# Performance work log

Measured on AMD Instinct MI355X. Metric: run time of the kernel, lower is better.

The kernel has to match this reference:

```python
import jax, jax.numpy as jnp
import numpy as np

N, P, C, T, V = 32, 6, 128, 64, 25
S = 3        # num_subset
CI = 32      # inter_channels
EPS = 1e-5
NEG_SLOPE = 0.1


def conv1x1(x, w, b):
    # x: (N,P,Cin,T,V), w: (Cout,Cin), b: (Cout,)
    return jnp.einsum('npctv,oc->npotv', x, w) + b[None, None, :, None, None]


def batchnorm(x, gamma, beta):
    # training-mode BN over (N,P,T,V) per channel, matching torch forward math
    mu = x.mean(axis=(0, 1, 3, 4), keepdims=True)
    var = x.var(axis=(0, 1, 3, 4), keepdims=True)
    xh = (x - mu) * jax.lax.rsqrt(var + EPS)
    return xh * gamma[None, None, :, None, None] + beta[None, None, :, None, None]


def leaky(x):
    return jnp.where(x >= 0, x, NEG_SLOPE * x)


def t_block(inp, att_bias, alphat, w_in, b_in, w_out, b_out, g_out, be_out,
            w_ff, b_ff, g_ff, be_ff):
    n, p, c, t, v = inp.shape
    qk = conv1x1(inp, w_in, b_in)                       # (N,P,2*S*CI,T,V)
    qk = qk.reshape(n, p, 2, S, CI, t, v).transpose(2, 0, 3, 1, 4, 5, 6)
    q, k = qk[0], qk[1]                                 # (N,S,P,CI,T,V)
    scores = jnp.einsum('nspctv,nspcqv->nsptq', q, k) / (CI * v)
    att = att_bias + jnp.tanh(scores) * alphat          # (N,S,P,T,T)
    y = jnp.einsum('npctv,nsptq->nspcqv', inp, att)     # (N,S,P,C,T,V)
    y = y.transpose(0, 2, 1, 3, 4, 5).reshape(n, p, S * c, t, v)
    y = batchnorm(conv1x1(y, w_out, b_out), g_out, be_out)
    y = leaky(inp + y)                                  # residual (identity down path)
    y2 = batchnorm(conv1x1(y, w_ff, b_ff), g_ff, be_ff)
    return leaky(y + y2)


def setup_inputs() -> dict:
    key = jax.random.key(0)
    ks = jax.random.split(key, 8)
    sc = 0.05
    return {
        'x': jax.random.normal(ks[0], (N, P, C, T, V), jnp.float32),
        'att_t1': jnp.zeros((1, S, 1, T, T), jnp.float32),
        'att_t2': jnp.zeros((1, S, 1, T, T), jnp.float32),
        'alphat': jnp.ones((1, S, 1, 1, 1), jnp.float32),
        'w_in': jax.random.normal(ks[1], (2 * S * CI, C), jnp.float32) * sc,
        'b_in': jax.random.normal(ks[2], (2 * S * CI,), jnp.float32) * sc,
        'w_out': jax.random.normal(ks[3], (C, S * C), jnp.float32) * sc,
        'b_out': jax.random.normal(ks[4], (C,), jnp.float32) * sc,
        'g_out': jnp.ones((C,), jnp.float32),
        'be_out': jnp.zeros((C,), jnp.float32),
        'w_ff': jax.random.normal(ks[5], (C, C), jnp.float32) * sc,
        'b_ff': jax.random.normal(ks[6], (C,), jnp.float32) * sc,
        'g_ff': jnp.ones((C,), jnp.float32),
        'be_ff': jnp.zeros((C,), jnp.float32),
    }


def reference(x, att_t1, att_t2, alphat, w_in, b_in, w_out, b_out, g_out,
              be_out, w_ff, b_ff, g_ff, be_ff):
    y = t_block(x, att_t1, alphat, w_in, b_in, w_out, b_out, g_out, be_out,
                w_ff, b_ff, g_ff, be_ff)
    z = t_block(y, att_t2, alphat, w_in, b_in, w_out, b_out, g_out, be_out,
                w_ff, b_ff, g_ff, be_ff)
    return z
```

## Files before the change

### kernel.cpp

```cpp
#include <hip/hip_runtime.h>
#include <hip/hip_bf16.h>
#include <math.h>

#define NPB  192
#define CCH  128
#define TT   64
#define VV   25
#define PIX  1600
#define SS   3
#define EPC  307200.0f
static const size_t ETOT = (size_t)NPB * CCH * PIX;

typedef __attribute__((ext_vector_type(4))) float f32x4;
typedef __attribute__((ext_vector_type(8))) short short8;

__device__ __forceinline__ ushort f2bf(float f) {
    __hip_bfloat16 h = __float2bfloat16(f);
    return __builtin_bit_cast(unsigned short, h);
}
__device__ __forceinline__ float bf2f(ushort u) {
    unsigned int x = ((unsigned int)u) << 16;
    return __builtin_bit_cast(float, x);
}

__global__ void wprep(const float* __restrict__ w_in, const float* __restrict__ b_in,
                      const float* __restrict__ w_out, const float* __restrict__ w_ff,
                      ushort* __restrict__ Wp, float* __restrict__ bp,
                      ushort* __restrict__ Wo, ushort* __restrict__ Wf) {
    int i = blockIdx.x * 256 + threadIdx.x;
    if (i < 192 * 128) {
        int r = i >> 7, c = i & 127;
        int s = r / 64, j = r % 64;
        int src = (j < 32) ? (s * 32 + j) : (96 + s * 32 + (j - 32));
        Wp[i] = f2bf(w_in[src * 128 + c]);
        if (c == 0) bp[r] = b_in[src];
    }
    if (i < 128 * 384) Wo[i] = f2bf(w_out[i]);
    if (i < 128 * 128) Wf[i] = f2bf(w_ff[i]);
}

__global__ void remap_x(const float* __restrict__ x, ushort* __restrict__ xr) {
    size_t o = ((size_t)blockIdx.x * 256 + threadIdx.x) * 4;
    size_t row = o / PIX;
    int p = (int)(o % PIX);
    int v = p >> 6, t0 = p & 63;
    const float* xp = x + row * PIX;
    uint2 u;
    u.x = (uint)f2bf(xp[(t0 + 0) * 25 + v]) | ((uint)f2bf(xp[(t0 + 1) * 25 + v]) << 16);
    u.y = (uint)f2bf(xp[(t0 + 2) * 25 + v]) | ((uint)f2bf(xp[(t0 + 3) * 25 + v]) << 16);
    *(uint2*)(xr + o) = u;
}

__global__ __launch_bounds__(256)
void gemm_conv(const void* __restrict__ inp, int in_bf16,
               const ushort* __restrict__ W, int ldw,
               const float* __restrict__ bias,
               void* __restrict__ outp, int out_bf16, int out_ch,
               int accflag)
{
    __shared__ ushort Wt[64 * 72];
    __shared__ ushort Xt[128 * 72];
    const int np = blockIdx.x;
    const int pixbase = blockIdx.y * 128;
    const int obase = blockIdx.z * 64;
    const int tid = threadIdx.x;
    const int wave = tid >> 6, lane = tid & 63;
    const int quad = lane >> 4, l16 = lane & 15;
    const int wPix = wave * 32;

    f32x4 acc[4][2];
    if (accflag) {
        const float* op = (const float*)outp + ((size_t)np * out_ch + obase) * PIX + pixbase;
#pragma unroll
        for (int ms = 0; ms < 4; ++ms)
#pragma unroll
            for (int ns = 0; ns < 2; ++ns) {
                int pl = wPix + ns * 16 + l16;
                bool valid = (pixbase + pl) < PIX;
#pragma unroll
                for (int r = 0; r < 4; ++r) {
                    int ol = ms * 16 + quad * 4 + r;
                    acc[ms][ns][r] = valid ? op[(size_t)ol * PIX + pl] : 0.f;
                }
            }
    } else {
#pragma unroll
        for (int ms = 0; ms < 4; ++ms) {
            float bv[4];
#pragma unroll
            for (int r = 0; r < 4; ++r) {
                int ol = ms * 16 + quad * 4 + r;
                bv[r] = bias ? bias[obase + ol] : 0.f;
            }
#pragma unroll
            for (int ns = 0; ns < 2; ++ns)
#pragma unroll
                for (int r = 0; r < 4; ++r) acc[ms][ns][r] = bv[r];
        }
    }

    const ushort* inb = (const ushort*)inp;
    const float* inf = (const float*)inp;
    const size_t in_off = (size_t)np * 128 * PIX;

    for (int kc = 0; kc < 2; ++kc) {
        const int kbase = kc * 64;
        {
            int o = tid >> 2, seg = tid & 3;
            const ushort* src = W + (size_t)(obase + o) * ldw + kbase + seg * 16;
            uint4 a = *(const uint4*)src;
            uint4 b = *(const uint4*)(src + 8);
            *(uint4*)&Wt[o * 72 + seg * 16] = a;
            *(uint4*)&Wt[o * 72 + seg * 16 + 8] = b;
        }
        {
            int cp = tid & 31, rq = tid >> 5;
            int c = cp * 2;
            int p0 = rq * 16;
            bool valid = (pixbase + p0) < PIX;
            if (in_bf16) {
                uint ra[8], rb[8];
                if (valid) {
                    const ushort* s0 = inb + in_off + (size_t)(kbase + c) * PIX + pixbase + p0;
                    const ushort* s1 = s0 + PIX;
                    *(uint4*)&ra[0] = *(const uint4*)s0;
                    *(uint4*)&ra[4] = *(const uint4*)(s0 + 8);
                    *(uint4*)&rb[0] = *(const uint4*)s1;
                    *(uint4*)&rb[4] = *(const uint4*)(s1 + 8);
                } else {
#pragma unroll
                    for (int h = 0; h < 8; ++h) { ra[h] = 0; rb[h] = 0; }
                }
#pragma unroll
                for (int h = 0; h < 8; ++h) {
                    uint lo = ra[h], hi = rb[h];
                    *(uint*)&Xt[(p0 + 2 * h) * 72 + c] = (lo & 0xffffu) | (hi << 16);
                    *(uint*)&Xt[(p0 + 2 * h + 1) * 72 + c] = (lo >> 16) | (hi & 0xffff0000u);
                }
            } else {
                if (valid) {
                    const float* s0 = inf + in_off + (size_t)(kbase + c) * PIX + pixbase + p0;
                    const float* s1 = s0 + PIX;
#pragma unroll
                    for (int b4 = 0; b4 < 4; ++b4) {
                        float4 u = ((const float4*)s0)[b4];
                        float4 w4 = ((const float4*)s1)[b4];
                        int p = p0 + b4 * 4;
                        *(uint*)&Xt[(p + 0) * 72 + c] = (uint)f2bf(u.x) | ((uint)f2bf(w4.x) << 16);
                        *(uint*)&Xt[(p + 1) * 72 + c] = (uint)f2bf(u.y) | ((uint)f2bf(w4.y) << 16);
                        *(uint*)&Xt[(p + 2) * 72 + c] = (uint)f2bf(u.z) | ((uint)f2bf(w4.z) << 16);
                        *(uint*)&Xt[(p + 3) * 72 + c] = (uint)f2bf(u.w) | ((uint)f2bf(w4.w) << 16);
                    }
                } else {
#pragma unroll
                    for (int h = 0; h < 16; ++h) *(uint*)&Xt[(p0 + h) * 72 + c] = 0;
                }
            }
        }
        __syncthreads();
#pragma unroll
        for (int ks = 0; ks < 2; ++ks) {
            const int kk = ks * 32;
            short8 a[4], b[2];
#pragma unroll
            for (int ms = 0; ms < 4; ++ms)
                a[ms] = *(const short8*)&Wt[(ms * 16 + l16) * 72 + kk + quad * 8];
#pragma unroll
            for (int ns = 0; ns < 2; ++ns)
                b[ns] = *(const short8*)&Xt[(wPix + ns * 16 + l16) * 72 + kk + quad * 8];
#pragma unroll
            for (int ms = 0; ms < 4; ++ms)
#pragma unroll
                for (int ns = 0; ns < 2; ++ns)
                    acc[ms][ns] = __builtin_amdgcn_mfma_f32_16x16x32_bf16(a[ms], b[ns], acc[ms][ns], 0, 0, 0);
        }
        __syncthreads();
    }

    if (out_bf16) {
        ushort* op = (ushort*)outp + ((size_t)np * out_ch + obase) * PIX + pixbase;
#pragma unroll
        for (int ms = 0; ms < 4; ++ms)
#pragma unroll
            for (int ns = 0; ns < 2; ++ns) {
                int pl = wPix + ns * 16 + l16;
                if (pixbase + pl >= PIX) continue;
#pragma unroll
                for (int r = 0; r < 4; ++r) {
                    int ol = ms * 16 + quad * 4 + r;
                    op[(size_t)ol * PIX + pl] = f2bf(acc[ms][ns][r]);
                }
            }
    } else {
        float* op = (float*)outp + ((size_t)np * out_ch + obase) * PIX + pixbase;
#pragma unroll
        for (int ms = 0; ms < 4; ++ms)
#pragma unroll
            for (int ns = 0; ns < 2; ++ns) {
                int pl = wPix + ns * 16 + l16;
                if (pixbase + pl >= PIX) continue;
#pragma unroll
                for (int r = 0; r < 4; ++r) {
                    int ol = ms * 16 + quad * 4 + r;
                    op[(size_t)ol * PIX + pl] = acc[ms][ns][r];
                }
            }
    }
}

__global__ __launch_bounds__(256)
void scores_mfma(const ushort* __restrict__ qk, const float* __restrict__ attb,
                 const float* __restrict__ alphat, ushort* __restrict__ attq)
{
    __shared__ ushort Qs[64 * 128];
    __shared__ ushort Ks[64 * 128];
    const int np = blockIdx.x, s = blockIdx.y, tid = threadIdx.x;
    const int wave = tid >> 6, lane = tid & 63;
    const int quad = lane >> 4, l16 = lane & 15;
    const int qW = (wave >> 1) * 32, tW = (wave & 1) * 32;
    const ushort* qb = qk + ((size_t)np * 192 + s * 64) * PIX;
    const ushort* kb = qb + (size_t)32 * PIX;

    const int side = wave >> 1;
    const int cil = (wave & 1) * 2 + (lane >> 5);
    const int t0 = (lane & 31) * 2;
    const ushort* sbase = (side ? kb : qb);
    ushort* dst = side ? Ks : Qs;

    f32x4 acc[2][2];
#pragma unroll
    for (int ms = 0; ms < 2; ++ms)
#pragma unroll
        for (int ns = 0; ns < 2; ++ns)
#pragma unroll
            for (int r = 0; r < 4; ++r) acc[ms][ns][r] = 0.f;

    for (int c = 0; c < 8; ++c) {
        __syncthreads();
        {
            const int ci = c * 4 + cil;
            const ushort* sb = sbase + (size_t)ci * PIX + t0;
            uint u[25];
#pragma unroll
            for (int v = 0; v < 25; ++v)
                u[v] = *(const uint*)(sb + v * 64);
            uint rA[16], rB[16];
#pragma unroll
            for (int w2 = 0; w2 < 12; ++w2) {
                uint a = u[2 * w2], b = u[2 * w2 + 1];
                rA[w2] = (a & 0xffffu) | (b << 16);
                rB[w2] = (a >> 16) | (b & 0xffff0000u);
            }
            rA[12] = u[24] & 0xffffu;  rB[12] = u[24] >> 16;
            rA[13] = 0u; rA[14] = 0u; rA[15] = 0u;
            rB[13] = 0u; rB[14] = 0u; rB[15] = 0u;
#pragma unroll
            for (int b4 = 0; b4 < 4; ++b4) {
                int blkA = (cil * 4 + b4) ^ (t0 & 7);
                int blkB = (cil * 4 + b4) ^ ((t0 + 1) & 7);
                uint4 wa, wb;
                wa.x = rA[b4 * 4 + 0]; wa.y = rA[b4 * 4 + 1];
                wa.z = rA[b4 * 4 + 2]; wa.w = rA[b4 * 4 + 3];
                wb.x = rB[b4 * 4 + 0]; wb.y = rB[b4 * 4 + 1];
                wb.z = rB[b4 * 4 + 2]; wb.w = rB[b4 * 4 + 3];
                *(uint4*)&dst[t0 * 128 + blkA * 8] = wa;
                *(uint4*)&dst[(t0 + 1) * 128 + blkB * 8] = wb;
            }
        }
        __syncthreads();
#pragma unroll
        for (int ks = 0; ks < 4; ++ks) {
            short8 a[2], b[2];
#pragma unroll
            for (int ms = 0; ms < 2; ++ms) {
                int q = qW + ms * 16 + l16;
                int blk = (ks * 4 + quad) ^ (q & 7);
                a[ms] = *(const short8*)&Ks[q * 128 + blk * 8];
            }
#pragma unroll
            for (int ns = 0; ns < 2; ++ns) {
                int t = tW + ns * 16 + l16;
                int blk = (ks * 4 + quad) ^ (t & 7);
                b[ns] = *(const short8*)&Qs[t * 128 + blk * 8];
            }
#pragma unroll
            for (int ms = 0; ms < 2; ++ms)
#pragma unroll
                for (int ns = 0; ns < 2; ++ns)
                    acc[ms][ns] = __builtin_amdgcn_mfma_f32_16x16x32_bf16(a[ms], b[ns], acc[ms][ns], 0, 0, 0);
        }
    }

    const float alpha = alphat[s];
    const int n = np / 6, p = np % 6;
    const float* bp2 = attb + (size_t)s * 4096;
    ushort* ap = attq + ((size_t)(n * SS + s) * 6 + p) * 4096;
    const float inv = 1.0f / 800.0f;
#pragma unroll
    for (int ms = 0; ms < 2; ++ms)
#pragma unroll
        for (int ns = 0; ns < 2; ++ns) {
            int t = tW + ns * 16 + l16;
#pragma unroll
            for (int r = 0; r < 4; ++r) {
                int q = qW + ms * 16 + quad * 4 + r;
                ap[q * 64 + t] = f2bf(bp2[t * 64 + q] + tanhf(acc[ms][ns][r] * inv) * alpha);
            }
        }
}

__global__ __launch_bounds__(256, 4)
void attn_conv(const ushort* __restrict__ xr, const ushort* __restrict__ attq,
               const ushort* __restrict__ Wo, const float* __restrict__ bias,
               float* __restrict__ Z)
{
    __shared__ ushort Xa[128 * 64];
    __shared__ ushort Ta[64 * 64];
    __shared__ ushort Ys[64 * 128];
    const int np = blockIdx.x, v = blockIdx.y;
    const int tid = threadIdx.x;
    const int wave = tid >> 6, lane = tid & 63;
    const int quad = lane >> 4, l16 = lane & 15;
    const int mH = (wave & 1) * 64;
    const int oH = (wave & 1) * 64;
    const int qH = (wave >> 1) * 32;
    const int n = np / 6, p = np % 6;

    {
        int cc = tid >> 1, half = tid & 1;
        const ushort* src = xr + ((size_t)np * 128 + cc) * PIX + v * 64 + half * 32;
        uint4 a = *(const uint4*)src;
        uint4 b = *(const uint4*)(src + 8);
        uint4 c0 = *(const uint4*)(src + 16);
        uint4 d = *(const uint4*)(src + 24);
        int sw = cc & 7;
        ushort* xb = &Xa[cc * 64];
        *(uint4*)&xb[((half * 4 + 0) ^ sw) * 8] = a;
        *(uint4*)&xb[((half * 4 + 1) ^ sw) * 8] = b;
        *(uint4*)&xb[((half * 4 + 2) ^ sw) * 8] = c0;
        *(uint4*)&xb[((half * 4 + 3) ^ sw) * 8] = d;
    }

    f32x4 acc2[4][2];
#pragma unroll
    for (int ms2 = 0; ms2 < 4; ++ms2) {
        float bv[4];
#pragma unroll
        for (int r = 0; r < 4; ++r)
            bv[r] = bias[oH + ms2 * 16 + quad * 4 + r];
#pragma unroll
        for (int ns = 0; ns < 2; ++ns)
#pragma unroll
            for (int r = 0; r < 4; ++r) acc2[ms2][ns][r] = bv[r];
    }

    const size_t abase = ((size_t)(n * SS) * 6 + p) * 4096;

    for (int s = 0; s < SS; ++s) {
        __syncthreads();
        {
            int r0 = tid >> 2, seg = tid & 3;
            const ushort* src = attq + abase + (size_t)s * 6 * 4096 + r0 * 64 + seg * 16;
            uint4 a = *(const uint4*)src;
            uint4 b = *(const uint4*)(src + 8);
            int sw = r0 & 7;
            ushort* tb = &Ta[r0 * 64];
            *(uint4*)&tb[((seg * 2 + 0) ^ sw) * 8] = a;
            *(uint4*)&tb[((seg * 2 + 1) ^ sw) * 8] = b;
        }
        __syncthreads();
        f32x4 acc[4][2];
#pragma unroll
        for (int ms = 0; ms < 4; ++ms)
#pragma unroll
            for (int ns = 0; ns < 2; ++ns)
#pragma unroll
                for (int r = 0; r < 4; ++r) acc[ms][ns][r] = 0.f;
#pragma unroll
        for (int ks = 0; ks < 2; ++ks) {
            short8 a[4], b[2];
#pragma unroll
            for (int ms = 0; ms < 4; ++ms) {
                int row = mH + ms * 16 + l16;
                int blk = (ks * 4 + quad) ^ (l16 & 7);
                a[ms] = *(const short8*)&Xa[row * 64 + blk * 8];
            }
#pragma unroll
            for (int ns = 0; ns < 2; ++ns) {
                int row = qH + ns * 16 + l16;
                int blk = (ks * 4 + quad) ^ (l16 & 7);
                b[ns] = *(const short8*)&Ta[row * 64 + blk * 8];
            }
#pragma unroll
            for (int ms = 0; ms < 4; ++ms)
#pragma unroll
                for (int ns = 0; ns < 2; ++ns)
                    acc[ms][ns] = __builtin_amdgcn_mfma_f32_16x16x32_bf16(a[ms], b[ns], acc[ms][ns], 0, 0, 0);
        }
#pragma unroll
        for (int ms = 0; ms < 4; ++ms)
#pragma unroll
            for (int ns = 0; ns < 2; ++ns) {
                int q = qH + ns * 16 + l16;
                int c0 = mH + ms * 16 + quad * 4;
                uint w0 = (uint)f2bf(acc[ms][ns][0]) | ((uint)f2bf(acc[ms][ns][1]) << 16);
                uint w1 = (uint)f2bf(acc[ms][ns][2]) | ((uint)f2bf(acc[ms][ns][3]) << 16);
                int blk = (c0 >> 3) ^ (q & 7);
                ushort* d = &Ys[q * 128 + blk * 8 + (c0 & 7)];
                *(uint*)d = w0;
                *(uint*)(d + 2) = w1;
            }
        __syncthreads();
#pragma unroll
        for (int ks2 = 0; ks2 < 4; ++ks2) {
            short8 wfa[4];
            const ushort* wb = Wo + (size_t)(oH + l16) * 384 + s * 128 + ks2 * 32 + quad * 8;
#pragma unroll
            for (int ms2 = 0; ms2 < 4; ++ms2)
                wfa[ms2] = *(const short8*)(wb + (size_t)ms2 * 16 * 384);
            short8 b2[2];
#pragma unroll
            for (int ns = 0; ns < 2; ++ns) {
                int q = qH + ns * 16 + l16;
                int blk = (ks2 * 4 + quad) ^ (q & 7);
                b2[ns] = *(const short8*)&Ys[q * 128 + blk * 8];
            }
#pragma unroll
            for (int ms2 = 0; ms2 < 4; ++ms2)
#pragma unroll
                for (int ns = 0; ns < 2; ++ns)
                    acc2[ms2][ns] = __builtin_amdgcn_mfma_f32_16x16x32_bf16(wfa[ms2], b2[ns], acc2[ms2][ns], 0, 0, 0);
        }
    }

    float* zp = Z + (size_t)np * 128 * PIX + v * 64;
#pragma unroll
    for (int ms2 = 0; ms2 < 4; ++ms2)
#pragma unroll
        for (int ns = 0; ns < 2; ++ns) {
            int q = qH + ns * 16 + l16;
#pragma unroll
            for (int r = 0; r < 4; ++r) {
                int o = oH + ms2 * 16 + quad * 4 + r;
                zp[(size_t)o * PIX + q] = acc2[ms2][ns][r];
            }
        }
}

__global__ void bn_stats(const float* __restrict__ z, float* __restrict__ stats) {
    const int c = blockIdx.x, np = blockIdx.y, tid = threadIdx.x;
    const float* zp = z + ((size_t)np * CCH + c) * PIX;
    float s = 0.f, s2 = 0.f;
    for (int i = tid; i < PIX; i += 256) {
        float v = zp[i];
        s += v; s2 += v * v;
    }
    for (int off = 32; off; off >>= 1) {
        s += __shfl_down(s, off);
        s2 += __shfl_down(s2, off);
    }
    __shared__ float ls[4], ls2[4];
    const int w = tid >> 6, lane = tid & 63;
    if (lane == 0) { ls[w] = s; ls2[w] = s2; }
    __syncthreads();
    if (tid == 0) {
        s = ls[0] + ls[1] + ls[2] + ls[3];
        s2 = ls2[0] + ls2[1] + ls2[2] + ls2[3];
        atomicAdd(&stats[c], s);
        atomicAdd(&stats[128 + c], s2);
    }
}

__global__ void bn_finalize(const float* __restrict__ stats, const float* __restrict__ g,
                            const float* __restrict__ be, float* __restrict__ scsh) {
    const int c = threadIdx.x;
    float mean = stats[c] * (1.0f / EPC);
    float var = stats[128 + c] * (1.0f / EPC) - mean * mean;
    float inv = rsqrtf(var + 1e-5f);
    float sc = g[c] * inv;
    scsh[c] = sc;
    scsh[128 + c] = be[c] - mean * sc;
}

__global__ void res_bn_g(const float* __restrict__ x, const float* __restrict__ z,
                         const float* __restrict__ scsh, float* __restrict__ out,
                         ushort* __restrict__ outb) {
    size_t i = ((size_t)blockIdx.x * 256 + threadIdx.x) * 4;
    size_t row = i / PIX;
    int p = (int)(i % PIX);
    int ch = (int)(row & 127);
    float sc = scsh[ch], sh = scsh[128 + ch];
    const float* zr = z + row * PIX;
    float4 a = *(const float4*)(x + i);
    float xin[4] = {a.x, a.y, a.z, a.w};
    float4 r;
    float ro[4];
#pragma unroll
    for (int j = 0; j < 4; ++j) {
        int pp = p + j;
        int t = pp / 25, vv = pp - t * 25;
        float zz = zr[vv * 64 + t];
        float val = xin[j] + fmaf(zz, sc, sh);
        ro[j] = val >= 0.f ? val : 0.1f * val;
    }
    r.x = ro[0]; r.y = ro[1]; r.z = ro[2]; r.w = ro[3];
    *(float4*)(out + i) = r;
    uint2 ub;
    ub.x = (uint)f2bf(ro[0]) | ((uint)f2bf(ro[1]) << 16);
    ub.y = (uint)f2bf(ro[2]) | ((uint)f2bf(ro[3]) << 16);
    *(uint2*)(outb + i) = ub;
}

__global__ void res_bn_l(const float4* __restrict__ xr, const float4* __restrict__ zr,
                         const float* __restrict__ scsh, float4* __restrict__ out) {
    int i = blockIdx.x * 256 + threadIdx.x;
    int row = i / 400;
    int ch = row & 127;
    float sc = scsh[ch], sh = scsh[128 + ch];
    float4 a = xr[i], b = zr[i], r;
    r.x = a.x + fmaf(b.x, sc, sh);
    r.y = a.y + fmaf(b.y, sc, sh);
    r.z = a.z + fmaf(b.z, sc, sh);
    r.w = a.w + fmaf(b.w, sc, sh);
    r.x = r.x >= 0.f ? r.x : 0.1f * r.x;
    r.y = r.y >= 0.f ? r.y : 0.1f * r.y;
    r.z = r.z >= 0.f ? r.z : 0.1f * r.z;
    r.w = r.w >= 0.f ? r.w : 0.1f * r.w;
    out[i] = r;
}

struct Ctx {
    ushort *xr, *Wp, *Wo, *Wf, *ATTQ;
    float *bp;
    float *R1, *R0, *STATS;
    const float *alphat, *b_out, *g_out, *be_out, *b_ff, *g_ff, *be_ff;
};

static void run_block(const float* X, const float* attb, float* OUT,
                      const Ctx& c, hipStream_t stream) {
    const int EG = 38400;
    remap_x<<<EG, 256, 0, stream>>>(X, c.xr);
    gemm_conv<<<dim3(NPB, 13, 3), 256, 0, stream>>>(c.xr, 1, c.Wp, 128, c.bp,
                                                    (void*)c.R1, 1, 192, 0);
    scores_mfma<<<dim3(NPB, 3), 256, 0, stream>>>((const ushort*)c.R1, attb, c.alphat, c.ATTQ);
    attn_conv<<<dim3(NPB, VV), 256, 0, stream>>>(c.xr, c.ATTQ, c.Wo, c.b_out, c.R0);
    hipMemsetAsync(c.STATS, 0, 256 * sizeof(float), stream);
    bn_stats<<<dim3(CCH, NPB), 256, 0, stream>>>(c.R0, c.STATS);
    bn_finalize<<<1, 128, 0, stream>>>(c.STATS, c.g_out, c.be_out, c.STATS + 256);
    res_bn_g<<<EG, 256, 0, stream>>>(X, c.R0, c.STATS + 256, c.R1, c.xr);
    gemm_conv<<<dim3(NPB, 13, 2), 256, 0, stream>>>(c.xr, 1, c.Wf, 128, c.b_ff,
                                                    (void*)c.R0, 0, 128, 0);
    hipMemsetAsync(c.STATS, 0, 256 * sizeof(float), stream);
    bn_stats<<<dim3(CCH, NPB), 256, 0, stream>>>(c.R0, c.STATS);
    bn_finalize<<<1, 128, 0, stream>>>(c.STATS, c.g_ff, c.be_ff, c.STATS + 256);
    res_bn_l<<<EG, 256, 0, stream>>>((const float4*)c.R1, (const float4*)c.R0,
                                     c.STATS + 256, (float4*)OUT);
}

extern "C" void kernel_launch(void* const* d_in, const int* in_sizes, int n_in,
                              void* d_out, int out_size, void* d_ws, size_t ws_size,
                              hipStream_t stream) {
    const float* x = (const float*)d_in[0];
    const float* att1 = (const float*)d_in[1];
    const float* att2 = (const float*)d_in[2];
    Ctx c;
    c.alphat = (const float*)d_in[3];
    const float* w_in = (const float*)d_in[4];
    const float* b_in = (const float*)d_in[5];
    const float* w_out = (const float*)d_in[6];
    c.b_out = (const float*)d_in[7];
    c.g_out = (const float*)d_in[8];
    c.be_out = (const float*)d_in[9];
    const float* w_ff = (const float*)d_in[10];
    c.b_ff = (const float*)d_in[11];
    c.g_ff = (const float*)d_in[12];
    c.be_ff = (const float*)d_in[13];

    char* ws = (char*)d_ws;
    size_t off = 0;
    c.xr = (ushort*)(ws + off);   off += ETOT * 2;
    c.R1 = (float*)(ws + off);    off += ETOT * 4;
    c.R0 = (float*)(ws + off);    off += ETOT * 4;
    c.ATTQ = (ushort*)(ws + off); off += (size_t)32 * 3 * 6 * 4096 * 2;
    c.STATS = (float*)(ws + off); off += 512 * 4;
    c.Wp = (ushort*)(ws + off);   off += 192 * 128 * 2;
    c.bp = (float*)(ws + off);    off += 192 * 4;
    c.Wo = (ushort*)(ws + off);   off += 128 * 384 * 2;
    c.Wf = (ushort*)(ws + off);   off += 128 * 128 * 2;

    wprep<<<192, 256, 0, stream>>>(w_in, b_in, w_out, w_ff, c.Wp, c.bp, c.Wo, c.Wf);

    float* out = (float*)d_out;
    run_block(x, att1, out, c, stream);
    run_block(out, att2, out, c, stream);
}
```

Measured before the change: 1.570 ms.

## Fuse BN statistics into conv epilogues and read attention tiles from global

Removes the standalone bn_stats kernel by computing per-channel sum and sum of squares in the epilogues of attn_conv and the feed-forward gemm_conv, using wave shuffles and atomics. This avoids re-reading the full fp32 conv outputs from memory twice per block. It also drops the LDS staging of the attention matrix in attn_conv and loads its B fragments straight from global memory, which removes two barriers per subset. The cost is many more float atomics on 256 addresses and uncoalesced global fragment loads in the inner loop, and the accflag accumulation path is removed.

```diff
diff --git a/kernel.cpp b/kernel.cpp
--- a/kernel.cpp
+++ b/kernel.cpp
@@ -56,7 +56,7 @@
                const ushort* __restrict__ W, int ldw,
                const float* __restrict__ bias,
                void* __restrict__ outp, int out_bf16, int out_ch,
-               int accflag)
+               float* __restrict__ stats)
 {
     __shared__ ushort Wt[64 * 72];
     __shared__ ushort Xt[128 * 72];
@@ -69,34 +69,18 @@
     const int wPix = wave * 32;
 
     f32x4 acc[4][2];
-    if (accflag) {
-        const float* op = (const float*)outp + ((size_t)np * out_ch + obase) * PIX + pixbase;
-#pragma unroll
-        for (int ms = 0; ms < 4; ++ms)
-#pragma unroll
-            for (int ns = 0; ns < 2; ++ns) {
-                int pl = wPix + ns * 16 + l16;
-                bool valid = (pixbase + pl) < PIX;
-#pragma unroll
-                for (int r = 0; r < 4; ++r) {
-                    int ol = ms * 16 + quad * 4 + r;
-                    acc[ms][ns][r] = valid ? op[(size_t)ol * PIX + pl] : 0.f;
-                }
-            }
-    } else {
-#pragma unroll
-        for (int ms = 0; ms < 4; ++ms) {
-            float bv[4];
-#pragma unroll
-            for (int r = 0; r < 4; ++r) {
-                int ol = ms * 16 + quad * 4 + r;
-                bv[r] = bias ? bias[obase + ol] : 0.f;
-            }
-#pragma unroll
-            for (int ns = 0; ns < 2; ++ns)
-#pragma unroll
-                for (int r = 0; r < 4; ++r) acc[ms][ns][r] = bv[r];
-        }
+#pragma unroll
+    for (int ms = 0; ms < 4; ++ms) {
+        float bv[4];
+#pragma unroll
+        for (int r = 0; r < 4; ++r) {
+            int ol = ms * 16 + quad * 4 + r;
+            bv[r] = bias ? bias[obase + ol] : 0.f;
+        }
+#pragma unroll
+        for (int ns = 0; ns < 2; ++ns)
+#pragma unroll
+            for (int r = 0; r < 4; ++r) acc[ms][ns][r] = bv[r];
     }
 
     const ushort* inb = (const ushort*)inp;
@@ -177,14 +161,19 @@
         __syncthreads();
     }
 
+    bool pv[2];
+#pragma unroll
+    for (int ns = 0; ns < 2; ++ns)
+        pv[ns] = (pixbase + wPix + ns * 16 + l16) < PIX;
+
     if (out_bf16) {
         ushort* op = (ushort*)outp + ((size_t)np * out_ch + obase) * PIX + pixbase;
 #pragma unroll
         for (int ms = 0; ms < 4; ++ms)
 #pragma unroll
             for (int ns = 0; ns < 2; ++ns) {
+                if (!pv[ns]) continue;
                 int pl = wPix + ns * 16 + l16;
-                if (pixbase + pl >= PIX) continue;
 #pragma unroll
                 for (int r = 0; r < 4; ++r) {
                     int ol = ms * 16 + quad * 4 + r;
@@ -197,12 +186,38 @@
         for (int ms = 0; ms < 4; ++ms)
 #pragma unroll
             for (int ns = 0; ns < 2; ++ns) {
+                if (!pv[ns]) continue;
                 int pl = wPix + ns * 16 + l16;
-                if (pixbase + pl >= PIX) continue;
 #pragma unroll
                 for (int r = 0; r < 4; ++r) {
                     int ol = ms * 16 + quad * 4 + r;
                     op[(size_t)ol * PIX + pl] = acc[ms][ns][r];
+                }
+            }
+    }
+
+    if (stats) {
+#pragma unroll
+        for (int ms = 0; ms < 4; ++ms)
+#pragma unroll
+            for (int r = 0; r < 4; ++r) {
+                float sv = 0.f, sq = 0.f;
+#pragma unroll
+                for (int ns = 0; ns < 2; ++ns) {
+                    if (pv[ns]) {
+                        float z = acc[ms][ns][r];
+                        sv += z; sq += z * z;
+                    }
+                }
+#pragma unroll
+                for (int m = 1; m < 16; m <<= 1) {
+                    sv += __shfl_xor(sv, m);
+                    sq += __shfl_xor(sq, m);
+                }
+                if (l16 == 0) {
+                    int ch = obase + ms * 16 + quad * 4 + r;
+                    atomicAdd(&stats[ch], sv);
+                    atomicAdd(&stats[128 + ch], sq);
                 }
             }
     }
@@ -312,10 +327,9 @@
 __global__ __launch_bounds__(256, 4)
 void attn_conv(const ushort* __restrict__ xr, const ushort* __restrict__ attq,
                const ushort* __restrict__ Wo, const float* __restrict__ bias,
-               float* __restrict__ Z)
+               float* __restrict__ Z, float* __restrict__ stats)
 {
     __shared__ ushort Xa[128 * 64];
-    __shared__ ushort Ta[64 * 64];
     __shared__ ushort Ys[64 * 128];
     const int np = blockIdx.x, v = blockIdx.y;
     const int tid = threadIdx.x;
@@ -354,21 +368,11 @@
             for (int r = 0; r < 4; ++r) acc2[ms2][ns][r] = bv[r];
     }
 
-    const size_t abase = ((size_t)(n * SS) * 6 + p) * 4096;
+    const ushort* tb0 = attq + ((size_t)(n * SS) * 6 + p) * 4096;
+    __syncthreads();
 
     for (int s = 0; s < SS; ++s) {
-        __syncthreads();
-        {
-            int r0 = tid >> 2, seg = tid & 3;
-            const ushort* src = attq + abase + (size_t)s * 6 * 4096 + r0 * 64 + seg * 16;
-            uint4 a = *(const uint4*)src;
-            uint4 b = *(const uint4*)(src + 8);
-            int sw = r0 & 7;
-            ushort* tb = &Ta[r0 * 64];
-            *(uint4*)&tb[((seg * 2 + 0) ^ sw) * 8] = a;
-            *(uint4*)&tb[((seg * 2 + 1) ^ sw) * 8] = b;
-        }
-        __syncthreads();
+        const ushort* ts = tb0 + (size_t)s * 6 * 4096;
         f32x4 acc[4][2];
 #pragma unroll
         for (int ms = 0; ms < 4; ++ms)
@@ -379,6 +383,9 @@
 #pragma unroll
         for (int ks = 0; ks < 2; ++ks) {
             short8 a[4], b[2];
+#pragma unroll
+            for (int ns = 0; ns < 2; ++ns)
+                b[ns] = *(const short8*)(ts + (size_t)(qH + ns * 16 + l16) * 64 + ks * 32 + quad * 8);
 #pragma unroll
             for (int ms = 0; ms < 4; ++ms) {
                 int row = mH + ms * 16 + l16;
@@ -386,17 +393,12 @@
                 a[ms] = *(const short8*)&Xa[row * 64 + blk * 8];
             }
 #pragma unroll
-            for (int ns = 0; ns < 2; ++ns) {
-                int row = qH + ns * 16 + l16;
-                int blk = (ks * 4 + quad) ^ (l16 & 7);
-                b[ns] = *(const short8*)&Ta[row * 64 + blk * 8];
-            }
-#pragma unroll
             for (int ms = 0; ms < 4; ++ms)
 #pragma unroll
                 for (int ns = 0; ns < 2; ++ns)
                     acc[ms][ns] = __builtin_amdgcn_mfma_f32_16x16x32_bf16(a[ms], b[ns], acc[ms][ns], 0, 0, 0);
         }
+        __syncthreads();
 #pragma unroll
         for (int ms = 0; ms < 4; ++ms)
 #pragma unroll
@@ -445,30 +447,24 @@
                 zp[(size_t)o * PIX + q] = acc2[ms2][ns][r];
             }
         }
-}
-
-__global__ void bn_stats(const float* __restrict__ z, float* __restrict__ stats) {
-    const int c = blockIdx.x, np = blockIdx.y, tid = threadIdx.x;
-    const float* zp = z + ((size_t)np * CCH + c) * PIX;
-    float s = 0.f, s2 = 0.f;
-    for (int i = tid; i < PIX; i += 256) {
-        float v = zp[i];
-        s += v; s2 += v * v;
-    }
-    for (int off = 32; off; off >>= 1) {
-        s += __shfl_down(s, off);
-        s2 += __shfl_down(s2, off);
-    }
-    __shared__ float ls[4], ls2[4];
-    const int w = tid >> 6, lane = tid & 63;
-    if (lane == 0) { ls[w] = s; ls2[w] = s2; }
-    __syncthreads();
-    if (tid == 0) {
-        s = ls[0] + ls[1] + ls[2] + ls[3];
-        s2 = ls2[0] + ls2[1] + ls2[2] + ls2[3];
-        atomicAdd(&stats[c], s);
-        atomicAdd(&stats[128 + c], s2);
-    }
+#pragma unroll
+    for (int ms2 = 0; ms2 < 4; ++ms2)
+#pragma unroll
+        for (int r = 0; r < 4; ++r) {
+            float sv = acc2[ms2][0][r] + acc2[ms2][1][r];
+            float sq = acc2[ms2][0][r] * acc2[ms2][0][r]
+                     + acc2[ms2][1][r] * acc2[ms2][1][r];
+#pragma unroll
+            for (int m = 1; m < 16; m <<= 1) {
+                sv += __shfl_xor(sv, m);
+                sq += __shfl_xor(sq, m);
+            }
+            if (l16 == 0) {
+                int o = oH + ms2 * 16 + quad * 4 + r;
+                atomicAdd(&stats[o], sv);
+                atomicAdd(&stats[128 + o], sq);
+            }
+        }
 }
 
 __global__ void bn_finalize(const float* __restrict__ stats, const float* __restrict__ g,
@@ -541,17 +537,16 @@
     const int EG = 38400;
     remap_x<<<EG, 256, 0, stream>>>(X, c.xr);
     gemm_conv<<<dim3(NPB, 13, 3), 256, 0, stream>>>(c.xr, 1, c.Wp, 128, c.bp,
-                                                    (void*)c.R1, 1, 192, 0);
+                                                    (void*)c.R1, 1, 192, nullptr);
     scores_mfma<<<dim3(NPB, 3), 256, 0, stream>>>((const ushort*)c.R1, attb, c.alphat, c.ATTQ);
-    attn_conv<<<dim3(NPB, VV), 256, 0, stream>>>(c.xr, c.ATTQ, c.Wo, c.b_out, c.R0);
     hipMemsetAsync(c.STATS, 0, 256 * sizeof(float), stream);
-    bn_stats<<<dim3(CCH, NPB), 256, 0, stream>>>(c.R0, c.STATS);
+    attn_conv<<<dim3(NPB, VV), 256, 0, stream>>>(c.xr, c.ATTQ, c.Wo, c.b_out,
+                                                 c.R0, c.STATS);
     bn_finalize<<<1, 128, 0, stream>>>(c.STATS, c.g_out, c.be_out, c.STATS + 256);
     res_bn_g<<<EG, 256, 0, stream>>>(X, c.R0, c.STATS + 256, c.R1, c.xr);
+    hipMemsetAsync(c.STATS, 0, 256 * sizeof(float), stream);
     gemm_conv<<<dim3(NPB, 13, 2), 256, 0, stream>>>(c.xr, 1, c.Wf, 128, c.b_ff,
-                                                    (void*)c.R0, 0, 128, 0);
-    hipMemsetAsync(c.STATS, 0, 256 * sizeof(float), stream);
-    bn_stats<<<dim3(CCH, NPB), 256, 0, stream>>>(c.R0, c.STATS);
+                                                    (void*)c.R0, 0, 128, c.STATS);
     bn_finalize<<<1, 128, 0, stream>>>(c.STATS, c.g_ff, c.be_ff, c.STATS + 256);
     res_bn_l<<<EG, 256, 0, stream>>>((const float4*)c.R1, (const float4*)c.R0,
                                      c.STATS + 256, (float4*)OUT);
```

New measurement: 5.525 ms. 3.52x slower.
